# Kernel tuning notes

Measured on AMD Instinct MI355X. Metric: run time of the kernel, lower is better.

The kernel has to match this reference:

```python
import jax, jax.numpy as jnp
import numpy as np

N, E = 50000, 800000
C, H = 64, 128  # out_channels, 2*out_channels


def gcn_conv(x, src, dst, W, b):
    # PyG GCNConv: h = x @ W; add self loops; sym-normalized sum aggregation; + bias
    n = x.shape[0]
    h = x @ W
    deg = jnp.zeros((n,), h.dtype).at[dst].add(1.0) + 1.0  # in-degree + self loop
    dinv = jax.lax.rsqrt(deg)
    norm = dinv[src] * dinv[dst]                            # [E]
    agg = jnp.zeros_like(h).at[dst].add(h[src] * norm[:, None])
    agg = agg + h * (1.0 / deg)[:, None]                    # self-loop term
    return agg + b


def setup_inputs() -> dict:
    key = jax.random.key(0)
    ks = jax.random.split(key, 12)
    g = lambda k, shp: (jax.random.normal(k, shp, jnp.float32) * 0.05)
    return {
        "x": jax.random.randint(ks[0], (N, 1), 0, 28),
        "edge_index": jax.random.randint(ks[1], (2, E), 0, N),
        "emb_W": g(ks[2], (28, H)),
        "W1": g(ks[3], (H, H)), "b1": jnp.zeros((H,), jnp.float32),
        "W2": g(ks[4], (H, H)), "b2": jnp.zeros((H,), jnp.float32),
        "W3": g(ks[5], (H, C)), "b3": jnp.zeros((C,), jnp.float32),
        "Wmu": g(ks[6], (C, C)), "bmu": jnp.zeros((C,), jnp.float32),
        "Wls": g(ks[7], (C, C)), "bls": jnp.zeros((C,), jnp.float32),
    }


def reference(x, edge_index, emb_W, W1, b1, W2, b2, W3, b3, Wmu, bmu, Wls, bls):
    src, dst = edge_index[0], edge_index[1]
    h = emb_W[x[:, 0]]                                      # [N, H] molecular embedding
    # PyG GCN(num_layers=3): ReLU between layers, none after last
    h = jax.nn.relu(gcn_conv(h, src, dst, W1, b1))
    h = jax.nn.relu(gcn_conv(h, src, dst, W2, b2))
    h = gcn_conv(h, src, dst, W3, b3)
    h = jax.nn.relu(h)                                      # .relu() in encoder forward
    mu = gcn_conv(h, src, dst, Wmu, bmu)
    logstd = gcn_conv(h, src, dst, Wls, bls)
    return (mu, logstd)
```

## Files before the change

kernel.cpp:

```cpp
#include <hip/hip_runtime.h>
#include <hip/hip_bf16.h>
#include <cstddef>



__global__ __launch_bounds__(256) void k_bcount(const int* __restrict__ dst,
                                                int* __restrict__ bcnt, int e) {
    __shared__ int h[256];
    const int tid = threadIdx.x;
    h[tid] = 0;
    __syncthreads();
    const int e0 = blockIdx.x * 4096;
    const int e1 = min(e0 + 4096, e);
    for (int j = e0 + tid; j < e1; j += 256) atomicAdd(&h[dst[j] >> 8], 1);
    __syncthreads();
    if (h[tid]) atomicAdd(&bcnt[tid], h[tid]);
}

__global__ __launch_bounds__(256) void k_bscan(const int* __restrict__ bcnt,
                                               int* __restrict__ boff) {
    __shared__ int wsum[4];
    const int tid = threadIdx.x;
    const int lane = tid & 63, wv = tid >> 6;
    int v0 = bcnt[tid];
    int v = v0;
#pragma unroll
    for (int d = 1; d < 64; d <<= 1) {
        int w = __shfl_up(v, d, 64);
        if (lane >= d) v += w;
    }
    if (lane == 63) wsum[wv] = v;
    __syncthreads();
    int woff = 0;
    for (int w = 0; w < wv; ++w) woff += wsum[w];
    int excl = woff + v - v0;
    boff[tid] = excl;
    if (tid == 255) boff[256] = excl + v0;
}

__global__ __launch_bounds__(256) void k_binA2(const int* __restrict__ src,
                                               const int* __restrict__ dst,
                                               const int* __restrict__ boff,
                                               int* __restrict__ gcur,
                                               int* __restrict__ packed,
                                               int e, int nb) {
    __shared__ int hist[256];
    __shared__ int base[256];
    __shared__ int bbase[256];
    const int tid = threadIdx.x;
    const int e0 = blockIdx.x * 4096;
    const int e1 = min(e0 + 4096, e);

    hist[tid] = 0;
    bbase[tid] = boff[tid];
    __syncthreads();
    for (int j = e0 + tid; j < e1; j += 256) atomicAdd(&hist[dst[j] >> 8], 1);
    __syncthreads();
    if (tid < nb && hist[tid] > 0) base[tid] = atomicAdd(&gcur[tid], hist[tid]);
    __syncthreads();
    hist[tid] = 0;
    __syncthreads();
    for (int j = e0 + tid; j < e1; j += 256) {
        int d = dst[j];
        int b = d >> 8;
        int r = atomicAdd(&hist[b], 1);
        packed[bbase[b] + base[b] + r] = ((d & 255) << 16) | src[j];
    }
}

#define BCAP 6144
__global__ __launch_bounds__(256) void k_binB2(const int* __restrict__ packed,
                                               const int* __restrict__ boff,
                                               const int* __restrict__ x,
                                               int* __restrict__ rptr,
                                               float* __restrict__ dinv,
                                               int2* __restrict__ xd,
                                               int* __restrict__ col,
                                               int n) {
    __shared__ int hist[256];
    __shared__ int cur[256];
    __shared__ int wsum[4];
    __shared__ int buf[BCAP];
    const int tid = threadIdx.x;
    const int lane = tid & 63, wv = tid >> 6;
    const int node0 = blockIdx.x << 8;
    const int node1 = min(node0 + 256, n);
    const int ebeg = boff[blockIdx.x];
    const int eend = boff[blockIdx.x + 1];
    const int cnt = eend - ebeg;

    hist[tid] = 0;
    __syncthreads();
    for (int j = tid; j < cnt; j += 256) atomicAdd(&hist[packed[ebeg + j] >> 16], 1);
    __syncthreads();
    const int deg = hist[tid];
    int v = deg;
#pragma unroll
    for (int d = 1; d < 64; d <<= 1) {
        int w = __shfl_up(v, d, 64);
        if (lane >= d) v += w;
    }
    if (lane == 63) wsum[wv] = v;
    __syncthreads();
    int woff = 0;
    for (int w = 0; w < wv; ++w) woff += wsum[w];
    const int excl = woff + v - deg;
    cur[tid] = excl;
    const int node = node0 + tid;
    if (node < node1) {
        rptr[node] = ebeg + excl;
        float dv = 1.0f / sqrtf((float)(deg + 1));
        dinv[node] = dv;
        xd[node] = make_int2(x[node], __float_as_int(dv));
    }
    if (node1 == n && tid == 0) rptr[n] = eend;
    __syncthreads();

    if (cnt <= BCAP) {
        for (int j = tid; j < cnt; j += 256) {
            int p = packed[ebeg + j];
            int pos = atomicAdd(&cur[p >> 16], 1);
            buf[pos] = p & 0xffff;
        }
        __syncthreads();
        for (int j = tid; j < cnt; j += 256) col[ebeg + j] = buf[j];
    } else {
        for (int j = tid; j < cnt; j += 256) {
            int p = packed[ebeg + j];
            int pos = atomicAdd(&cur[p >> 16], 1);
            col[ebeg + pos] = p & 0xffff;
        }
    }
}

__global__ __launch_bounds__(256) void k_smallmm(const float* __restrict__ embW,
                                                 const float* __restrict__ W1,
                                                 float* __restrict__ M, int V) {
    const int r = blockIdx.x * 2 + (threadIdx.x >> 7);
    const int c = threadIdx.x & 127;
    if (r >= V) return;
    float a0 = 0.f, a1 = 0.f;
    const float* er = embW + (size_t)r * 128;
#pragma unroll 4
    for (int k = 0; k < 128; k += 2) {
        a0 = fmaf(er[k], W1[(size_t)k * 128 + c], a0);
        a1 = fmaf(er[k + 1], W1[(size_t)(k + 1) * 128 + c], a1);
    }
    M[(size_t)r * 128 + c] = a0 + a1;
}

__global__ void k_catW(const float* __restrict__ Wmu, const float* __restrict__ Wls,
                       float* __restrict__ Wcat) {
    int i = blockIdx.x * 256 + threadIdx.x;
    if (i >= 64 * 128) return;
    int k = i >> 7, c = i & 127;
    Wcat[i] = (c < 64) ? Wmu[k * 64 + c] : Wls[k * 64 + (c - 64)];
}

__global__ __launch_bounds__(256) void k_gather_l1(const float* __restrict__ M,
                                                   const int* __restrict__ rptr,
                                                   const int* __restrict__ col,
                                                   const int2* __restrict__ xd,
                                                   const float* __restrict__ b,
                                                   float* __restrict__ out,
                                                   int n, int V) {
    __shared__ float sh[32 * 128];
    for (int f = threadIdx.x; f < V * 32; f += 256)
        ((float4*)sh)[f] = ((const float4*)M)[f];
    __syncthreads();

    const int wave = threadIdx.x >> 6;
    const int lane = threadIdx.x & 63;
    const int node = blockIdx.x * 4 + wave;
    if (node >= n) return;
    const int beg = rptr[node], end = rptr[node + 1];
    int j = beg;

    float ax0 = 0.f, ay0 = 0.f, ax1 = 0.f, ay1 = 0.f;
    const int lo = 2 * lane;
    if (end - beg >= 8) {
        int s[8];
#pragma unroll
        for (int u = 0; u < 8; ++u) s[u] = col[j + u];
        j += 8;
        while (true) {
            int2 p[8];
#pragma unroll
            for (int u = 0; u < 8; ++u) p[u] = xd[s[u]];
            const bool more = (j + 8 <= end);
            int sn[8];
            if (more) {
#pragma unroll
                for (int u = 0; u < 8; ++u) sn[u] = col[j + u];
            }
#pragma unroll
            for (int u = 0; u < 8; ++u) {
                float dv = __int_as_float(p[u].y);
                float2 v = *(const float2*)&sh[p[u].x * 128 + lo];
                if (u & 1) { ax1 = fmaf(dv, v.x, ax1); ay1 = fmaf(dv, v.y, ay1); }
                else       { ax0 = fmaf(dv, v.x, ax0); ay0 = fmaf(dv, v.y, ay0); }
            }
            if (!more) break;
#pragma unroll
            for (int u = 0; u < 8; ++u) s[u] = sn[u];
            j += 8;
        }
    }
    for (; j < end; ++j) {
        int2 p = xd[col[j]];
        float dv = __int_as_float(p.y);
        float2 v = *(const float2*)&sh[p.x * 128 + lo];
        ax0 = fmaf(dv, v.x, ax0); ay0 = fmaf(dv, v.y, ay0);
    }
    int2 pn = xd[node];
    float dn = __int_as_float(pn.y);
    float2 sv = *(const float2*)&sh[pn.x * 128 + lo];
    float2 bb = ((const float2*)b)[lane];
    float ox = (ax0 + ax1 + dn * sv.x) * dn + bb.x;
    float oy = (ay0 + ay1 + dn * sv.y) * dn + bb.y;
    ((float2*)out)[(size_t)node * 64 + lane] = {ox, oy};
}

template <int K, int COUT, bool RELU>
__global__ __launch_bounds__(256) void k_matmul(const float* __restrict__ in,
                                                const float* __restrict__ W,
                                                const float* __restrict__ dinv,
                                                float* __restrict__ out, int n) {
    constexpr int BM = 128, KC = 32, LDI = KC + 4;
    constexpr int CT = COUT / 16;
    __shared__ float sIn[BM * LDI];
    __shared__ float sW[KC * COUT];

    const int tid = threadIdx.x;
    const int row0 = blockIdx.x * BM;
    const int tc = tid & 15;
    const int tr = tid >> 4;

    float acc[8][CT];
#pragma unroll
    for (int j = 0; j < 8; ++j)
#pragma unroll
        for (int c = 0; c < CT; ++c) acc[j][c] = 0.f;

    const int sr = tid >> 3;
    const int sk = (tid & 7) * 4;

    for (int kc = 0; kc < K; kc += KC) {
#pragma unroll
        for (int p = 0; p < 4; ++p) {
            int rr = p * 32 + sr;
            int gr = row0 + rr;
            float4 v = {0.f, 0.f, 0.f, 0.f};
            if (gr < n) v = *(const float4*)&in[(size_t)gr * K + kc + sk];
            if (RELU) {
                v.x = fmaxf(v.x, 0.f); v.y = fmaxf(v.y, 0.f);
                v.z = fmaxf(v.z, 0.f); v.w = fmaxf(v.w, 0.f);
            }
            *(float4*)&sIn[rr * LDI + sk] = v;
        }
        for (int f4 = tid; f4 < KC * COUT / 4; f4 += 256)
            *(float4*)&sW[f4 * 4] = *(const float4*)&W[(size_t)kc * COUT + f4 * 4];
        __syncthreads();

        for (int kk = 0; kk < KC; kk += 4) {
            float4 a[8];
#pragma unroll
            for (int j = 0; j < 8; ++j)
                a[j] = *(const float4*)&sIn[(tr * 8 + j) * LDI + kk];
#pragma unroll
            for (int t = 0; t < 4; ++t) {
                float4 w0 = *(const float4*)&sW[(kk + t) * COUT + tc * 4];
                float4 w1;
                if constexpr (CT == 8)
                    w1 = *(const float4*)&sW[(kk + t) * COUT + COUT / 2 + tc * 4];
#pragma unroll
                for (int j = 0; j < 8; ++j) {
                    float av = (t == 0) ? a[j].x : (t == 1) ? a[j].y
                             : (t == 2) ? a[j].z : a[j].w;
                    acc[j][0] = fmaf(av, w0.x, acc[j][0]);
                    acc[j][1] = fmaf(av, w0.y, acc[j][1]);
                    acc[j][2] = fmaf(av, w0.z, acc[j][2]);
                    acc[j][3] = fmaf(av, w0.w, acc[j][3]);
                    if constexpr (CT == 8) {
                        acc[j][4] = fmaf(av, w1.x, acc[j][4]);
                        acc[j][5] = fmaf(av, w1.y, acc[j][5]);
                        acc[j][6] = fmaf(av, w1.z, acc[j][6]);
                        acc[j][7] = fmaf(av, w1.w, acc[j][7]);
                    }
                }
            }
        }
        __syncthreads();
    }

#pragma unroll
    for (int j = 0; j < 8; ++j) {
        int gr = row0 + tr * 8 + j;
        if (gr < n) {
            float dv = dinv[gr];
            float4 o0 = {acc[j][0] * dv, acc[j][1] * dv, acc[j][2] * dv, acc[j][3] * dv};
            *(float4*)&out[(size_t)gr * COUT + tc * 4] = o0;
            if constexpr (CT == 8) {
                float4 o1 = {acc[j][4] * dv, acc[j][5] * dv, acc[j][6] * dv, acc[j][7] * dv};
                *(float4*)&out[(size_t)gr * COUT + COUT / 2 + tc * 4] = o1;
            }
        }
    }
}

__global__ __launch_bounds__(256) void k_mm_heads(const float* __restrict__ in,
                                                  const float* __restrict__ W,
                                                  const float* __restrict__ bmu,
                                                  const float* __restrict__ bls,
                                                  float* __restrict__ mu,
                                                  float* __restrict__ ls, int n) {
    constexpr int BM = 128, KC = 32, LDI = KC + 4, K = 64, COUT = 128;
    __shared__ float sIn[BM * LDI];
    __shared__ float sW[KC * COUT];

    const int tid = threadIdx.x;
    const int row0 = blockIdx.x * BM;
    const int tc = tid & 15;
    const int tr = tid >> 4;

    float acc[8][8];
#pragma unroll
    for (int j = 0; j < 8; ++j)
#pragma unroll
        for (int c = 0; c < 8; ++c) acc[j][c] = 0.f;

    const int sr = tid >> 3;
    const int sk = (tid & 7) * 4;

    for (int kc = 0; kc < K; kc += KC) {
#pragma unroll
        for (int p = 0; p < 4; ++p) {
            int rr = p * 32 + sr;
            int gr = row0 + rr;
            float4 v = {0.f, 0.f, 0.f, 0.f};
            if (gr < n) v = *(const float4*)&in[(size_t)gr * K + kc + sk];
            *(float4*)&sIn[rr * LDI + sk] = v;
        }
        for (int f4 = tid; f4 < KC * COUT / 4; f4 += 256)
            *(float4*)&sW[f4 * 4] = *(const float4*)&W[(size_t)kc * COUT + f4 * 4];
        __syncthreads();

        for (int kk = 0; kk < KC; kk += 4) {
            float4 a[8];
#pragma unroll
            for (int j = 0; j < 8; ++j)
                a[j] = *(const float4*)&sIn[(tr * 8 + j) * LDI + kk];
#pragma unroll
            for (int t = 0; t < 4; ++t) {
                float4 w0 = *(const float4*)&sW[(kk + t) * COUT + tc * 4];
                float4 w1 = *(const float4*)&sW[(kk + t) * COUT + 64 + tc * 4];
#pragma unroll
                for (int j = 0; j < 8; ++j) {
                    float av = (t == 0) ? a[j].x : (t == 1) ? a[j].y
                             : (t == 2) ? a[j].z : a[j].w;
                    acc[j][0] = fmaf(av, w0.x, acc[j][0]);
                    acc[j][1] = fmaf(av, w0.y, acc[j][1]);
                    acc[j][2] = fmaf(av, w0.z, acc[j][2]);
                    acc[j][3] = fmaf(av, w0.w, acc[j][3]);
                    acc[j][4] = fmaf(av, w1.x, acc[j][4]);
                    acc[j][5] = fmaf(av, w1.y, acc[j][5]);
                    acc[j][6] = fmaf(av, w1.z, acc[j][6]);
                    acc[j][7] = fmaf(av, w1.w, acc[j][7]);
                }
            }
        }
        __syncthreads();
    }

    float4 bm = ((const float4*)bmu)[tc];
    float4 bl = ((const float4*)bls)[tc];
#pragma unroll
    for (int j = 0; j < 8; ++j) {
        int gr = row0 + tr * 8 + j;
        if (gr < n) {
            float4 o0 = {acc[j][0] + bm.x, acc[j][1] + bm.y, acc[j][2] + bm.z, acc[j][3] + bm.w};
            float4 o1 = {acc[j][4] + bl.x, acc[j][5] + bl.y, acc[j][6] + bl.z, acc[j][7] + bl.w};
            *(float4*)&mu[(size_t)gr * 64 + tc * 4] = o0;
            *(float4*)&ls[(size_t)gr * 64 + tc * 4] = o1;
        }
    }
}

__global__ __launch_bounds__(256) void k_gather128p(const float* __restrict__ tab,
                                                    const int* __restrict__ rptr,
                                                    const int* __restrict__ col,
                                                    const float* __restrict__ dinv,
                                                    const float* __restrict__ b,
                                                    float* __restrict__ out, int n) {
    const int wave = threadIdx.x >> 6;
    const int lane = threadIdx.x & 63;
    const int g = lane >> 5;
    const int q = lane & 31;
    const int node = blockIdx.x * 4 + wave;
    if (node >= n) return;
    const int beg = rptr[node], end = rptr[node + 1];

    float4 acc = {0.f, 0.f, 0.f, 0.f};
    int j = beg;
    if (j < end) {
        int s[8]; bool val[8];
#pragma unroll
        for (int u = 0; u < 8; ++u) {
            int ei = j + 2 * u + g;
            val[u] = ei < end;
            s[u] = val[u] ? col[ei] : node;
        }
        j += 16;
        while (true) {
            float4 v[8];
#pragma unroll
            for (int u = 0; u < 8; ++u)
                v[u] = *(const float4*)&tab[(size_t)s[u] * 128 + q * 4];
            const bool more = j < end;
            int sn[8]; bool vn[8];
            if (more) {
#pragma unroll
                for (int u = 0; u < 8; ++u) {
                    int ei = j + 2 * u + g;
                    vn[u] = ei < end;
                    sn[u] = vn[u] ? col[ei] : node;
                }
            }
#pragma unroll
            for (int u = 0; u < 8; ++u) {
                if (val[u]) {
                    acc.x += v[u].x; acc.y += v[u].y;
                    acc.z += v[u].z; acc.w += v[u].w;
                }
            }
            if (!more) break;
#pragma unroll
            for (int u = 0; u < 8; ++u) { s[u] = sn[u]; val[u] = vn[u]; }
            j += 16;
        }
    }
    acc.x += __shfl_xor(acc.x, 32, 64); acc.y += __shfl_xor(acc.y, 32, 64);
    acc.z += __shfl_xor(acc.z, 32, 64); acc.w += __shfl_xor(acc.w, 32, 64);

    if (g == 0) {
        float4 self = *(const float4*)&tab[(size_t)node * 128 + q * 4];
        float dn = dinv[node];
        float4 bb = ((const float4*)b)[q];
        float4 o = {(acc.x + self.x) * dn + bb.x, (acc.y + self.y) * dn + bb.y,
                    (acc.z + self.z) * dn + bb.z, (acc.w + self.w) * dn + bb.w};
        *(float4*)&out[(size_t)node * 128 + q * 4] = o;
    }
}

template <int MODE>
__global__ __launch_bounds__(256) void k_gather64p(const float* __restrict__ tab,
                                                   const int* __restrict__ rptr,
                                                   const int* __restrict__ col,
                                                   const float* __restrict__ dinv,
                                                   const float* __restrict__ b,
                                                   float* __restrict__ out, int n) {
    const int wave = threadIdx.x >> 6;
    const int lane = threadIdx.x & 63;
    const int g = lane >> 4;
    const int q = lane & 15;
    const int node = blockIdx.x * 4 + wave;
    if (node >= n) return;
    const int beg = rptr[node], end = rptr[node + 1];

    float4 acc = {0.f, 0.f, 0.f, 0.f};
    int j = beg;
    if (j < end) {
        int s[4]; bool val[4];
#pragma unroll
        for (int u = 0; u < 4; ++u) {
            int ei = j + 4 * u + g;
            val[u] = ei < end;
            s[u] = val[u] ? col[ei] : node;
        }
        j += 16;
        while (true) {
            float4 v[4];
#pragma unroll
            for (int u = 0; u < 4; ++u)
                v[u] = *(const float4*)&tab[(size_t)s[u] * 64 + q * 4];
            const bool more = j < end;
            int sn[4]; bool vn[4];
            if (more) {
#pragma unroll
                for (int u = 0; u < 4; ++u) {
                    int ei = j + 4 * u + g;
                    vn[u] = ei < end;
                    sn[u] = vn[u] ? col[ei] : node;
                }
            }
#pragma unroll
            for (int u = 0; u < 4; ++u) {
                if (val[u]) {
                    acc.x += v[u].x; acc.y += v[u].y;
                    acc.z += v[u].z; acc.w += v[u].w;
                }
            }
            if (!more) break;
#pragma unroll
            for (int u = 0; u < 4; ++u) { s[u] = sn[u]; val[u] = vn[u]; }
            j += 16;
        }
    }
    acc.x += __shfl_xor(acc.x, 16, 64); acc.y += __shfl_xor(acc.y, 16, 64);
    acc.z += __shfl_xor(acc.z, 16, 64); acc.w += __shfl_xor(acc.w, 16, 64);
    acc.x += __shfl_xor(acc.x, 32, 64); acc.y += __shfl_xor(acc.y, 32, 64);
    acc.z += __shfl_xor(acc.z, 32, 64); acc.w += __shfl_xor(acc.w, 32, 64);

    if (g == 0) {
        float4 self = *(const float4*)&tab[(size_t)node * 64 + q * 4];
        float dn = dinv[node];
        float4 o = {(acc.x + self.x) * dn, (acc.y + self.y) * dn,
                    (acc.z + self.z) * dn, (acc.w + self.w) * dn};
        if constexpr (MODE == 1) {
            float4 bb = ((const float4*)b)[q];
            o.x = fmaxf(o.x + bb.x, 0.f) * dn;
            o.y = fmaxf(o.y + bb.y, 0.f) * dn;
            o.z = fmaxf(o.z + bb.z, 0.f) * dn;
            o.w = fmaxf(o.w + bb.w, 0.f) * dn;
        }
        *(float4*)&out[(size_t)node * 64 + q * 4] = o;
    }
}

extern "C" void kernel_launch(void* const* d_in, const int* in_sizes, int n_in,
                              void* d_out, int out_size, void* d_ws, size_t ws_size,
                              hipStream_t stream) {
    const int*   x    = (const int*)d_in[0];
    const int*   ei   = (const int*)d_in[1];
    const float* embW = (const float*)d_in[2];
    const float* W1   = (const float*)d_in[3];
    const float* b1   = (const float*)d_in[4];
    const float* W2   = (const float*)d_in[5];
    const float* b2   = (const float*)d_in[6];
    const float* W3   = (const float*)d_in[7];
    const float* b3   = (const float*)d_in[8];
    const float* Wmu  = (const float*)d_in[9];
    const float* bmu  = (const float*)d_in[10];
    const float* Wls  = (const float*)d_in[11];
    const float* bls  = (const float*)d_in[12];

    const int n = in_sizes[0];
    const int e = in_sizes[1] / 2;
    const int V = in_sizes[2] / 128;
    const int* src = ei;
    const int* dst = ei + e;

    char* w = (char*)d_ws;
    auto alloc = [&](size_t bytes) {
        char* p = w;
        w += (bytes + 255) & ~(size_t)255;
        return p;
    };
    float* bufA = (float*)alloc((size_t)n * 128 * 4);
    float* bufB = (float*)alloc((size_t)n * 128 * 4);
    float* hW   = (float*)alloc((size_t)n * 128 * 4);
    int*   rptr = (int*)alloc((size_t)(n + 1) * 4);
    int*   col  = (int*)alloc((size_t)e * 4);
    int*   pck  = (int*)alloc((size_t)e * 4);
    float* dinv = (float*)alloc((size_t)n * 4);
    int2*  xd   = (int2*)alloc((size_t)n * 8);
    float* Wcat = (float*)alloc((size_t)64 * 128 * 4);
    float* Msm  = (float*)alloc((size_t)32 * 128 * 4);
    int*   bcnt = (int*)alloc((size_t)256 * 4);
    int*   boff = (int*)alloc((size_t)257 * 4);
    int*   gcur = (int*)alloc((size_t)256 * 4);

    const int nbuck = (n + 255) / 256;
    const int ntile = (e + 4095) / 4096;

    hipMemsetAsync(bcnt, 0, (size_t)256 * 4, stream);
    hipMemsetAsync(gcur, 0, (size_t)256 * 4, stream);
    k_bcount<<<ntile, 256, 0, stream>>>(dst, bcnt, e);
    k_bscan <<<1, 256, 0, stream>>>(bcnt, boff);
    k_binA2 <<<ntile, 256, 0, stream>>>(src, dst, boff, gcur, pck, e, nbuck);
    k_binB2 <<<nbuck, 256, 0, stream>>>(pck, boff, x, rptr, dinv, xd, col, n);
    k_smallmm<<<(V + 1) / 2, 256, 0, stream>>>(embW, W1, Msm, V);
    k_catW <<<(64 * 128 + 255) / 256, 256, 0, stream>>>(Wmu, Wls, Wcat);

    const int gmm = (n + 127) / 128;
    const int ggt = (n + 3) / 4;
    float* mu = (float*)d_out;
    float* ls = (float*)d_out + (size_t)n * 64;

    k_gather_l1<<<ggt, 256, 0, stream>>>(Msm, rptr, col, xd, b1, bufA, n, V);
    k_matmul<128, 128, true><<<gmm, 256, 0, stream>>>(bufA, W2, dinv, hW, n);
    k_gather128p<<<ggt, 256, 0, stream>>>(hW, rptr, col, dinv, b2, bufB, n);
    k_matmul<128, 64, true><<<gmm, 256, 0, stream>>>(bufB, W3, dinv, hW, n);
    k_gather64p<1><<<ggt, 256, 0, stream>>>(hW, rptr, col, dinv, b3, bufA, n);
    k_gather64p<2><<<ggt, 256, 0, stream>>>(bufA, rptr, col, dinv, bmu, bufB, n);
    k_mm_heads<<<gmm, 256, 0, stream>>>(bufB, Wcat, bmu, bls, mu, ls, n);
}
```

Measured before the change: 285.3 us.

## Fuse head gather with mu/logstd matmul and drop global atomics from binning

The final aggregation for the two output heads now runs in the same kernel as the 64x64 head matmuls. Each wave aggregates a node, then multiplies the result against an interleaved Wmu/Wls pair held in shared memory, so the intermediate buffer is never written and read back. Edge binning now stores a histogram per tile and does a per-tile prefix scan, which replaces the global atomic cursor and the memsets and makes the packed order deterministic. The small weight-prep kernels are merged into one launch. The risks are the serial scan over tiles in a single block and lower gather parallelism at 8 nodes per wave.

```diff
diff --git a/kernel.cpp b/kernel.cpp
--- a/kernel.cpp
+++ b/kernel.cpp
@@ -4,8 +4,8 @@
 
 
 
-__global__ __launch_bounds__(256) void k_bcount(const int* __restrict__ dst,
-                                                int* __restrict__ bcnt, int e) {
+__global__ __launch_bounds__(256) void k_hist(const int* __restrict__ dst,
+                                              int* __restrict__ hist_g, int e) {
     __shared__ int h[256];
     const int tid = threadIdx.x;
     h[tid] = 0;
@@ -14,16 +14,22 @@
     const int e1 = min(e0 + 4096, e);
     for (int j = e0 + tid; j < e1; j += 256) atomicAdd(&h[dst[j] >> 8], 1);
     __syncthreads();
-    if (h[tid]) atomicAdd(&bcnt[tid], h[tid]);
-}
-
-__global__ __launch_bounds__(256) void k_bscan(const int* __restrict__ bcnt,
-                                               int* __restrict__ boff) {
+    hist_g[blockIdx.x * 256 + tid] = h[tid];
+}
+
+__global__ __launch_bounds__(256) void k_scan2(const int* __restrict__ hist_g,
+                                               int* __restrict__ tbase,
+                                               int* __restrict__ boff, int ntile) {
+    const int b = threadIdx.x;
+    int acc = 0;
+    for (int t = 0; t < ntile; ++t) {
+        int v = hist_g[t * 256 + b];
+        tbase[t * 256 + b] = acc;
+        acc += v;
+    }
     __shared__ int wsum[4];
-    const int tid = threadIdx.x;
-    const int lane = tid & 63, wv = tid >> 6;
-    int v0 = bcnt[tid];
-    int v = v0;
+    const int lane = b & 63, wv = b >> 6;
+    int v = acc;
 #pragma unroll
     for (int d = 1; d < 64; d <<= 1) {
         int w = __shfl_up(v, d, 64);
@@ -33,38 +39,29 @@
     __syncthreads();
     int woff = 0;
     for (int w = 0; w < wv; ++w) woff += wsum[w];
-    int excl = woff + v - v0;
-    boff[tid] = excl;
-    if (tid == 255) boff[256] = excl + v0;
-}
-
-__global__ __launch_bounds__(256) void k_binA2(const int* __restrict__ src,
+    int excl = woff + v - acc;
+    boff[b] = excl;
+    if (b == 255) boff[256] = excl + acc;
+}
+
+__global__ __launch_bounds__(256) void k_binA3(const int* __restrict__ src,
                                                const int* __restrict__ dst,
                                                const int* __restrict__ boff,
-                                               int* __restrict__ gcur,
-                                               int* __restrict__ packed,
-                                               int e, int nb) {
+                                               const int* __restrict__ tbase,
+                                               int* __restrict__ packed, int e) {
     __shared__ int hist[256];
     __shared__ int base[256];
-    __shared__ int bbase[256];
     const int tid = threadIdx.x;
     const int e0 = blockIdx.x * 4096;
     const int e1 = min(e0 + 4096, e);
-
     hist[tid] = 0;
-    bbase[tid] = boff[tid];
-    __syncthreads();
-    for (int j = e0 + tid; j < e1; j += 256) atomicAdd(&hist[dst[j] >> 8], 1);
-    __syncthreads();
-    if (tid < nb && hist[tid] > 0) base[tid] = atomicAdd(&gcur[tid], hist[tid]);
-    __syncthreads();
-    hist[tid] = 0;
+    base[tid] = boff[tid] + tbase[blockIdx.x * 256 + tid];
     __syncthreads();
     for (int j = e0 + tid; j < e1; j += 256) {
         int d = dst[j];
         int b = d >> 8;
         int r = atomicAdd(&hist[b], 1);
-        packed[bbase[b] + base[b] + r] = ((d & 255) << 16) | src[j];
+        packed[base[b] + r] = ((d & 255) << 16) | src[j];
     }
 }
 
@@ -133,28 +130,29 @@
     }
 }
 
-__global__ __launch_bounds__(256) void k_smallmm(const float* __restrict__ embW,
-                                                 const float* __restrict__ W1,
-                                                 float* __restrict__ M, int V) {
-    const int r = blockIdx.x * 2 + (threadIdx.x >> 7);
-    const int c = threadIdx.x & 127;
-    if (r >= V) return;
-    float a0 = 0.f, a1 = 0.f;
-    const float* er = embW + (size_t)r * 128;
+__global__ __launch_bounds__(256) void k_prepW(const float* __restrict__ embW,
+                                               const float* __restrict__ W1,
+                                               const float* __restrict__ Wmu,
+                                               const float* __restrict__ Wls,
+                                               float* __restrict__ M,
+                                               float2* __restrict__ Wpair,
+                                               int V, int nsm) {
+    if ((int)blockIdx.x < nsm) {
+        const int r = blockIdx.x * 2 + (threadIdx.x >> 7);
+        const int c = threadIdx.x & 127;
+        if (r >= V) return;
+        float a0 = 0.f, a1 = 0.f;
+        const float* er = embW + (size_t)r * 128;
 #pragma unroll 4
-    for (int k = 0; k < 128; k += 2) {
-        a0 = fmaf(er[k], W1[(size_t)k * 128 + c], a0);
-        a1 = fmaf(er[k + 1], W1[(size_t)(k + 1) * 128 + c], a1);
-    }
-    M[(size_t)r * 128 + c] = a0 + a1;
-}
-
-__global__ void k_catW(const float* __restrict__ Wmu, const float* __restrict__ Wls,
-                       float* __restrict__ Wcat) {
-    int i = blockIdx.x * 256 + threadIdx.x;
-    if (i >= 64 * 128) return;
-    int k = i >> 7, c = i & 127;
-    Wcat[i] = (c < 64) ? Wmu[k * 64 + c] : Wls[k * 64 + (c - 64)];
+        for (int k = 0; k < 128; k += 2) {
+            a0 = fmaf(er[k], W1[(size_t)k * 128 + c], a0);
+            a1 = fmaf(er[k + 1], W1[(size_t)(k + 1) * 128 + c], a1);
+        }
+        M[(size_t)r * 128 + c] = a0 + a1;
+    } else {
+        int i = (blockIdx.x - nsm) * 256 + threadIdx.x;
+        if (i < 64 * 64) Wpair[i] = make_float2(Wmu[i], Wls[i]);
+    }
 }
 
 __global__ __launch_bounds__(256) void k_gather_l1(const float* __restrict__ M,
@@ -308,84 +306,6 @@
     }
 }
 
-__global__ __launch_bounds__(256) void k_mm_heads(const float* __restrict__ in,
-                                                  const float* __restrict__ W,
-                                                  const float* __restrict__ bmu,
-                                                  const float* __restrict__ bls,
-                                                  float* __restrict__ mu,
-                                                  float* __restrict__ ls, int n) {
-    constexpr int BM = 128, KC = 32, LDI = KC + 4, K = 64, COUT = 128;
-    __shared__ float sIn[BM * LDI];
-    __shared__ float sW[KC * COUT];
-
-    const int tid = threadIdx.x;
-    const int row0 = blockIdx.x * BM;
-    const int tc = tid & 15;
-    const int tr = tid >> 4;
-
-    float acc[8][8];
-#pragma unroll
-    for (int j = 0; j < 8; ++j)
-#pragma unroll
-        for (int c = 0; c < 8; ++c) acc[j][c] = 0.f;
-
-    const int sr = tid >> 3;
-    const int sk = (tid & 7) * 4;
-
-    for (int kc = 0; kc < K; kc += KC) {
-#pragma unroll
-        for (int p = 0; p < 4; ++p) {
-            int rr = p * 32 + sr;
-            int gr = row0 + rr;
-            float4 v = {0.f, 0.f, 0.f, 0.f};
-            if (gr < n) v = *(const float4*)&in[(size_t)gr * K + kc + sk];
-            *(float4*)&sIn[rr * LDI + sk] = v;
-        }
-        for (int f4 = tid; f4 < KC * COUT / 4; f4 += 256)
-            *(float4*)&sW[f4 * 4] = *(const float4*)&W[(size_t)kc * COUT + f4 * 4];
-        __syncthreads();
-
-        for (int kk = 0; kk < KC; kk += 4) {
-            float4 a[8];
-#pragma unroll
-            for (int j = 0; j < 8; ++j)
-                a[j] = *(const float4*)&sIn[(tr * 8 + j) * LDI + kk];
-#pragma unroll
-            for (int t = 0; t < 4; ++t) {
-                float4 w0 = *(const float4*)&sW[(kk + t) * COUT + tc * 4];
-                float4 w1 = *(const float4*)&sW[(kk + t) * COUT + 64 + tc * 4];
-#pragma unroll
-                for (int j = 0; j < 8; ++j) {
-                    float av = (t == 0) ? a[j].x : (t == 1) ? a[j].y
-                             : (t == 2) ? a[j].z : a[j].w;
-                    acc[j][0] = fmaf(av, w0.x, acc[j][0]);
-                    acc[j][1] = fmaf(av, w0.y, acc[j][1]);
-                    acc[j][2] = fmaf(av, w0.z, acc[j][2]);
-                    acc[j][3] = fmaf(av, w0.w, acc[j][3]);
-                    acc[j][4] = fmaf(av, w1.x, acc[j][4]);
-                    acc[j][5] = fmaf(av, w1.y, acc[j][5]);
-                    acc[j][6] = fmaf(av, w1.z, acc[j][6]);
-                    acc[j][7] = fmaf(av, w1.w, acc[j][7]);
-                }
-            }
-        }
-        __syncthreads();
-    }
-
-    float4 bm = ((const float4*)bmu)[tc];
-    float4 bl = ((const float4*)bls)[tc];
-#pragma unroll
-    for (int j = 0; j < 8; ++j) {
-        int gr = row0 + tr * 8 + j;
-        if (gr < n) {
-            float4 o0 = {acc[j][0] + bm.x, acc[j][1] + bm.y, acc[j][2] + bm.z, acc[j][3] + bm.w};
-            float4 o1 = {acc[j][4] + bl.x, acc[j][5] + bl.y, acc[j][6] + bl.z, acc[j][7] + bl.w};
-            *(float4*)&mu[(size_t)gr * 64 + tc * 4] = o0;
-            *(float4*)&ls[(size_t)gr * 64 + tc * 4] = o1;
-        }
-    }
-}
-
 __global__ __launch_bounds__(256) void k_gather128p(const float* __restrict__ tab,
                                                     const int* __restrict__ rptr,
                                                     const int* __restrict__ col,
@@ -452,7 +372,6 @@
     }
 }
 
-template <int MODE>
 __global__ __launch_bounds__(256) void k_gather64p(const float* __restrict__ tab,
                                                    const int* __restrict__ rptr,
                                                    const int* __restrict__ col,
@@ -514,16 +433,111 @@
     if (g == 0) {
         float4 self = *(const float4*)&tab[(size_t)node * 64 + q * 4];
         float dn = dinv[node];
+        float4 bb = ((const float4*)b)[q];
         float4 o = {(acc.x + self.x) * dn, (acc.y + self.y) * dn,
                     (acc.z + self.z) * dn, (acc.w + self.w) * dn};
-        if constexpr (MODE == 1) {
-            float4 bb = ((const float4*)b)[q];
-            o.x = fmaxf(o.x + bb.x, 0.f) * dn;
-            o.y = fmaxf(o.y + bb.y, 0.f) * dn;
-            o.z = fmaxf(o.z + bb.z, 0.f) * dn;
-            o.w = fmaxf(o.w + bb.w, 0.f) * dn;
-        }
+        o.x = fmaxf(o.x + bb.x, 0.f) * dn;
+        o.y = fmaxf(o.y + bb.y, 0.f) * dn;
+        o.z = fmaxf(o.z + bb.z, 0.f) * dn;
+        o.w = fmaxf(o.w + bb.w, 0.f) * dn;
         *(float4*)&out[(size_t)node * 64 + q * 4] = o;
+    }
+}
+
+__global__ __launch_bounds__(256) void k_gather_heads(const float* __restrict__ tab,
+                                                      const int* __restrict__ rptr,
+                                                      const int* __restrict__ col,
+                                                      const float* __restrict__ dinv,
+                                                      const float* __restrict__ bmu,
+                                                      const float* __restrict__ bls,
+                                                      const float2* __restrict__ Wpair,
+                                                      float* __restrict__ mu,
+                                                      float* __restrict__ ls, int n) {
+    __shared__ float2 wp[64 * 64];
+    for (int f = threadIdx.x; f < 64 * 64 / 2; f += 256)
+        ((float4*)wp)[f] = ((const float4*)Wpair)[f];
+    __syncthreads();
+
+    const int wave = threadIdx.x >> 6;
+    const int lane = threadIdx.x & 63;
+    const int g = lane >> 4;
+    const int q = lane & 15;
+    const float bmu_c = bmu[lane];
+    const float bls_c = bls[lane];
+
+    for (int i = 0; i < 8; ++i) {
+        const int node = blockIdx.x * 32 + wave * 8 + i;
+        if (node >= n) break;
+        const int beg = rptr[node], end = rptr[node + 1];
+
+        float4 acc = {0.f, 0.f, 0.f, 0.f};
+        int j = beg;
+        if (j < end) {
+            int s[4]; bool val[4];
+#pragma unroll
+            for (int u = 0; u < 4; ++u) {
+                int ei = j + 4 * u + g;
+                val[u] = ei < end;
+                s[u] = val[u] ? col[ei] : node;
+            }
+            j += 16;
+            while (true) {
+                float4 v[4];
+#pragma unroll
+                for (int u = 0; u < 4; ++u)
+                    v[u] = *(const float4*)&tab[(size_t)s[u] * 64 + q * 4];
+                const bool more = j < end;
+                int sn[4]; bool vn[4];
+                if (more) {
+#pragma unroll
+                    for (int u = 0; u < 4; ++u) {
+                        int ei = j + 4 * u + g;
+                        vn[u] = ei < end;
+                        sn[u] = vn[u] ? col[ei] : node;
+                    }
+                }
+#pragma unroll
+                for (int u = 0; u < 4; ++u) {
+                    if (val[u]) {
+                        acc.x += v[u].x; acc.y += v[u].y;
+                        acc.z += v[u].z; acc.w += v[u].w;
+                    }
+                }
+                if (!more) break;
+#pragma unroll
+                for (int u = 0; u < 4; ++u) { s[u] = sn[u]; val[u] = vn[u]; }
+                j += 16;
+            }
+        }
+        acc.x += __shfl_xor(acc.x, 16, 64); acc.y += __shfl_xor(acc.y, 16, 64);
+        acc.z += __shfl_xor(acc.z, 16, 64); acc.w += __shfl_xor(acc.w, 16, 64);
+        acc.x += __shfl_xor(acc.x, 32, 64); acc.y += __shfl_xor(acc.y, 32, 64);
+        acc.z += __shfl_xor(acc.z, 32, 64); acc.w += __shfl_xor(acc.w, 32, 64);
+
+        const float dn = dinv[node];
+        float4 self = *(const float4*)&tab[(size_t)node * 64 + q * 4];
+        float4 o = {(acc.x + self.x) * dn, (acc.y + self.y) * dn,
+                    (acc.z + self.z) * dn, (acc.w + self.w) * dn};
+
+        float am = 0.f, al = 0.f;
+#pragma unroll
+        for (int qq = 0; qq < 16; ++qq) {
+            float r0 = __shfl(o.x, qq, 64);
+            float r1 = __shfl(o.y, qq, 64);
+            float r2 = __shfl(o.z, qq, 64);
+            float r3 = __shfl(o.w, qq, 64);
+            const int k0 = qq * 4;
+            float2 w0 = wp[(k0 + 0) * 64 + lane];
+            float2 w1 = wp[(k0 + 1) * 64 + lane];
+            float2 w2 = wp[(k0 + 2) * 64 + lane];
+            float2 w3 = wp[(k0 + 3) * 64 + lane];
+            am = fmaf(r0, w0.x, am); al = fmaf(r0, w0.y, al);
+            am = fmaf(r1, w1.x, am); al = fmaf(r1, w1.y, al);
+            am = fmaf(r2, w2.x, am); al = fmaf(r2, w2.y, al);
+            am = fmaf(r3, w3.x, am); al = fmaf(r3, w3.y, al);
+        }
+        mu[(size_t)node * 64 + lane] = am + bmu_c;
+        ls[(size_t)node * 64 + lane] = al + bls_c;
     }
 }
 
@@ -564,23 +578,22 @@
     int*   pck  = (int*)alloc((size_t)e * 4);
     float* dinv = (float*)alloc((size_t)n * 4);
     int2*  xd   = (int2*)alloc((size_t)n * 8);
-    float* Wcat = (float*)alloc((size_t)64 * 128 * 4);
+    float2* Wpr = (float2*)alloc((size_t)64 * 64 * 8);
     float* Msm  = (float*)alloc((size_t)32 * 128 * 4);
-    int*   bcnt = (int*)alloc((size_t)256 * 4);
     int*   boff = (int*)alloc((size_t)257 * 4);
-    int*   gcur = (int*)alloc((size_t)256 * 4);
-
+
+    const int ntile = (e + 4095) / 4096;
     const int nbuck = (n + 255) / 256;
-    const int ntile = (e + 4095) / 4096;
-
-    hipMemsetAsync(bcnt, 0, (size_t)256 * 4, stream);
-    hipMemsetAsync(gcur, 0, (size_t)256 * 4, stream);
-    k_bcount<<<ntile, 256, 0, stream>>>(dst, bcnt, e);
-    k_bscan <<<1, 256, 0, stream>>>(bcnt, boff);
-    k_binA2 <<<ntile, 256, 0, stream>>>(src, dst, boff, gcur, pck, e, nbuck);
-    k_binB2 <<<nbuck, 256, 0, stream>>>(pck, boff, x, rptr, dinv, xd, col, n);
-    k_smallmm<<<(V + 1) / 2, 256, 0, stream>>>(embW, W1, Msm, V);
-    k_catW <<<(64 * 128 + 255) / 256, 256, 0, stream>>>(Wmu, Wls, Wcat);
+    int* hist_g = (int*)alloc((size_t)ntile * 256 * 4);
+    int* tbase  = (int*)alloc((size_t)ntile * 256 * 4);
+
+    const int nsm = (V + 1) / 2;
+
+    k_hist <<<ntile, 256, 0, stream>>>(dst, hist_g, e);
+    k_scan2<<<1, 256, 0, stream>>>(hist_g, tbase, boff, ntile);
+    k_binA3<<<ntile, 256, 0, stream>>>(src, dst, boff, tbase, pck, e);
+    k_binB2<<<nbuck, 256, 0, stream>>>(pck, boff, x, rptr, dinv, xd, col, n);
+    k_prepW<<<nsm + 16, 256, 0, stream>>>(embW, W1, Wmu, Wls, Msm, Wpr, V, nsm);
 
     const int gmm = (n + 127) / 128;
     const int ggt = (n + 3) / 4;
@@ -591,7 +604,7 @@
     k_matmul<128, 128, true><<<gmm, 256, 0, stream>>>(bufA, W2, dinv, hW, n);
     k_gather128p<<<ggt, 256, 0, stream>>>(hW, rptr, col, dinv, b2, bufB, n);
     k_matmul<128, 64, true><<<gmm, 256, 0, stream>>>(bufB, W3, dinv, hW, n);
-    k_gather64p<1><<<ggt, 256, 0, stream>>>(hW, rptr, col, dinv, b3, bufA, n);
-    k_gather64p<2><<<ggt, 256, 0, stream>>>(bufA, rptr, col, dinv, bmu, bufB, n);
-    k_mm_heads<<<gmm, 256, 0, stream>>>(bufB, Wcat, bmu, bls, mu, ls, n);
-}
+    k_gather64p<<<ggt, 256, 0, stream>>>(hW, rptr, col, dinv, b3, bufA, n);
+    k_gather_heads<<<(n + 31) / 32, 256, 0, stream>>>(bufA, rptr, col, dinv,
+                                                      bmu, bls, Wpr, mu, ls, n);
+}
```

New measurement: 344.0 us. 1.21x slower.
